# Kernel optimization log

Hardware: AMD Instinct MI355X
Metric: run time of the kernel (lower is better)

Reference implementation:

```python
import jax, jax.numpy as jnp
import numpy as np

_EPS = 1e-5
RC = 5.0   # cutoff radius
L = 20     # number of radial basis functions
N = 10000  # nodes
E = 100000 # edges
F = 128    # in_feats


def _ssp(x):
    # ShiftedSoftplus: softplus(x) - log(2)
    return jax.nn.softplus(x) - jnp.log(2.0)


def _rbf(r):
    # DimeNet radial basis: sqrt(2/rc) * sin(n*pi*r/rc) / r, n = 1..L.  r: [E,1] -> [E,L]
    n = jnp.arange(1, L + 1, dtype=r.dtype)
    return jnp.sqrt(2.0 / RC) * jnp.sin(n * jnp.pi * r / RC) / r


def _fc(u):
    # cosine cutoff applied elementwise: 0.5*(cos(pi*u/rc)+1) for u < rc else 0
    return jnp.where(u < RC, 0.5 * (jnp.cos(jnp.pi * u / RC) + 1.0), 0.0)


def setup_inputs() -> dict:
    key = jax.random.key(0)
    ks = jax.random.split(key, 12)

    def nrm(k, shape, scale=1.0):
        return jax.random.normal(k, shape, dtype=jnp.float32) * scale

    return {
        "x": nrm(ks[0], (N, 3)) * 3.0,           # atomic positions
        "v": nrm(ks[1], (N, F, 3)),               # vector node features
        "s": nrm(ks[2], (N, F)),                  # scalar node features
        "ms1_w": nrm(ks[3], (F, F), F ** -0.5),
        "ms1_b": jnp.zeros((F,), jnp.float32),
        "ms2_w": nrm(ks[4], (3 * F, F), F ** -0.5),
        "ms2_b": jnp.zeros((3 * F,), jnp.float32),
        "mv_w": nrm(ks[5], (3 * F, L), L ** -0.5),
        "mv_b": jnp.zeros((3 * F,), jnp.float32),
        "us1_w": nrm(ks[6], (F, F), F ** -0.5),
        "us1_b": jnp.zeros((F,), jnp.float32),
        "us2_w": nrm(ks[7], (3 * F, F), F ** -0.5),
        "us2_b": jnp.zeros((3 * F,), jnp.float32),
        "src": jax.random.randint(ks[8], (E,), 0, N, dtype=jnp.int32),
        "dst": jax.random.randint(ks[9], (E,), 0, N, dtype=jnp.int32),
    }


def reference(x, v, s, ms1_w, ms1_b, ms2_w, ms2_b, mv_w, mv_b,
              us1_w, us1_b, us2_w, us2_b, src, dst):
    # ---------- pass 1: message1 + reduce1 (sum over incoming edges) ----------
    sj = s[src]                                   # [E,F]   src scalar features
    vj = v[src]                                   # [E,F,3] src vector features
    vec = x[src] - x[dst]                         # [E,3]   x_i - x_j (molecule branch)
    r = jnp.sqrt(jnp.sum(vec ** 2, axis=-1) + _EPS)[:, None]          # [E,1]
    phi = _ssp(sj @ ms1_w.T + ms1_b) @ ms2_w.T + ms2_b                 # [E,3F]
    w = _fc(_rbf(r) @ mv_w.T + mv_b)                                    # [E,3F]
    v_, s_, r_ = jnp.split(phi * w, 3, axis=-1)                         # each [E,F]
    dv_e = vj * v_[:, :, None] + r_[:, :, None] * (vec / r)[:, None, :] # [E,F,3]
    dv = jax.ops.segment_sum(dv_e, dst, num_segments=N)                 # [N,F,3]
    ds = jax.ops.segment_sum(s_, dst, num_segments=N)                   # [N,F]
    v_new = v + dv
    s_new = s + ds

    # ---------- pass 2: message2 + reduce2 (mean over incoming edges) ----------
    s2 = _ssp(s_new[src] @ us1_w.T + us1_b) @ us2_w.T + us2_b           # [E,3F]
    deg = jax.ops.segment_sum(jnp.ones((E,), s.dtype), dst, num_segments=N)
    denom = jnp.maximum(deg, 1.0)
    s_mean = jax.ops.segment_sum(s2, dst, num_segments=N) / denom[:, None]        # [N,3F]
    uv = jax.ops.segment_sum(v_new[src], dst, num_segments=N) / denom[:, None, None]  # [N,F,3]
    avv, asv, ass = jnp.split(s_mean, 3, axis=-1)                       # each [N,F]
    norm = jnp.sqrt(jnp.sum(uv ** 2, axis=-1) + _EPS)[..., None]        # [N,F,1]
    dv2 = uv * avv[:, :, None]                                           # [N,F,3]
    ds2 = jnp.sum((uv / norm) ** 2, axis=-1) * asv + ass                 # [N,F]
    return (v_new + dv2, s_new + ds2)
```

## Files before the change

### kernel.cpp

```cpp
#include <hip/hip_runtime.h>
#include <hip/hip_bf16.h>


#define F_DIM   128
#define F3_DIM  384
#define L_DIM   20
#define CAP     64

typedef __attribute__((ext_vector_type(8))) short short8;
typedef __attribute__((ext_vector_type(4))) float f32x4;
typedef __attribute__((ext_vector_type(4))) unsigned short us4;

struct u3 { unsigned a, b, c; };

__device__ __forceinline__ unsigned short f2bf(float f) {
  union { float f; unsigned u; } a; a.f = f;
  unsigned u = a.u;
  u = (u + 0x7FFFu + ((u >> 16) & 1u)) >> 16;
  return (unsigned short)u;
}
__device__ __forceinline__ float bf2f(unsigned short u) {
  union { unsigned u; float f; } a; a.u = ((unsigned)u) << 16;
  return a.f;
}

__global__ __launch_bounds__(256) void cast_fill_kernel(
    const float* __restrict__ ms1_w, unsigned short* __restrict__ w_ms1,
    const float* __restrict__ ms2_w, unsigned short* __restrict__ w_ms2,
    const float* __restrict__ us1_w, unsigned short* __restrict__ w_us1,
    const float* __restrict__ us2_w, unsigned short* __restrict__ w_us2,
    const float* __restrict__ s,     unsigned short* __restrict__ sbf,
    const float* __restrict__ v,     us4* __restrict__ v4,
    const float* __restrict__ mv_w,  unsigned short* __restrict__ mvwB,
    const int* __restrict__ src, const int* __restrict__ dst,
    int* __restrict__ cursor, int* __restrict__ jbuf,
    int nF, int E)
{
  int i = blockIdx.x * 256 + threadIdx.x;
  if (i < 16384) w_ms1[i] = f2bf(ms1_w[i]);
  if (i < 49152) w_ms2[i] = f2bf(ms2_w[i]);
  if (i < 16384) w_us1[i] = f2bf(us1_w[i]);
  if (i < 49152) w_us2[i] = f2bf(us2_w[i]);
  if (i < nF)    sbf[i] = f2bf(s[i]);
  if (i < nF) {
    const float* vp = v + (size_t)i * 3;
    us4 o; o.x = f2bf(vp[0]); o.y = f2bf(vp[1]); o.z = f2bf(vp[2]); o.w = 0;
    v4[i] = o;
  }
  if (i < 384 * 32) {
    int o = i >> 5, k = i & 31;
    float val = (k < 20) ? mv_w[o * 20 + k] * 0.6324555320336759f : 0.f;
    mvwB[i] = f2bf(val);
  }
  if (i < E) {
    int d = dst[i];
    int p = atomicAdd(&cursor[d], 1);
    if (p < CAP) jbuf[d * CAP + p] = src[i];
  }
}

__global__ __launch_bounds__(64) void mlp_kernel(
    const unsigned short* __restrict__ X,
    const unsigned short* __restrict__ W1,
    const float* __restrict__ B1,
    const unsigned short* __restrict__ W2,
    const float* __restrict__ B2,
    const us4* __restrict__ Vin,
    unsigned short* __restrict__ Yc)
{
  __shared__ float HT[128 * 17];
  const int lane = threadIdx.x;
  const int c    = lane & 15;
  const int quad = lane >> 4;
  const int m0   = blockIdx.x * 16;

  f32x4 acc[8];
#pragma unroll
  for (int t = 0; t < 8; t++) acc[t] = (f32x4){0.f, 0.f, 0.f, 0.f};
#pragma unroll
  for (int kk = 0; kk < 4; kk++) {
    short8 a = *(const short8*)(X + (size_t)(m0 + c) * 128 + kk * 32 + quad * 8);
#pragma unroll
    for (int t = 0; t < 8; t++) {
      short8 b = *(const short8*)(W1 + (size_t)(t * 16 + c) * 128 + kk * 32 + quad * 8);
      acc[t] = __builtin_amdgcn_mfma_f32_16x16x32_bf16(a, b, acc[t], 0, 0, 0);
    }
  }
#pragma unroll
  for (int t = 0; t < 8; t++) {
    float bias = B1[t * 16 + c];
    int k = t * 16 + c;
#pragma unroll
    for (int r = 0; r < 4; r++) {
      float h = acc[t][r] + bias;
      float sp = (h > 15.f) ? h : log1pf(__expf(h));
      sp -= 0.69314718056f;
      HT[k * 17 + quad * 4 + r] = sp;
    }
  }
  __syncthreads();

  f32x4 acc2[3][8];
#pragma unroll
  for (int g = 0; g < 3; g++)
#pragma unroll
    for (int t = 0; t < 8; t++) acc2[g][t] = (f32x4){0.f, 0.f, 0.f, 0.f};
#pragma unroll
  for (int kk = 0; kk < 4; kk++) {
    short8 afr;
#pragma unroll
    for (int j = 0; j < 8; j++) {
      float hv = HT[(kk * 32 + quad * 8 + j) * 17 + c];
      afr[j] = (short)f2bf(hv);
    }
#pragma unroll
    for (int g = 0; g < 3; g++)
#pragma unroll
      for (int t = 0; t < 8; t++) {
        short8 b = *(const short8*)(W2 + (size_t)(g * 128 + t * 16 + c) * 128 + kk * 32 + quad * 8);
        acc2[g][t] = __builtin_amdgcn_mfma_f32_16x16x32_bf16(afr, b, acc2[g][t], 0, 0, 0);
      }
  }
#pragma unroll
  for (int t = 0; t < 8; t++) {
    int f = t * 16 + c;
    float b0 = B2[f], b1 = B2[128 + f], b2 = B2[256 + f];
#pragma unroll
    for (int r = 0; r < 4; r++) {
      int m = quad * 4 + r;
      us4 vv = Vin[(size_t)(m0 + m) * 128 + f];
      unsigned p0 = f2bf(acc2[0][t][r] + b0);
      unsigned p1 = f2bf(acc2[1][t][r] + b1);
      unsigned p2 = f2bf(acc2[2][t][r] + b2);
      u3 rec;
      rec.a = p0 | (p1 << 16);
      rec.b = p2 | ((unsigned)vv.x << 16);
      rec.c = (unsigned)vv.y | ((unsigned)vv.z << 16);
      *(u3*)(Yc + ((size_t)(m0 + m) * 128 + f) * 6) = rec;
    }
  }
}

__global__ __launch_bounds__(256, 4) void pass1_kernel(
    const float* __restrict__ x,
    const unsigned short* __restrict__ combo1,
    const float* __restrict__ v,
    const float* __restrict__ s,
    const unsigned short* __restrict__ mvwB,
    const float* __restrict__ mv_b,
    const int* __restrict__ jbuf,
    const int* __restrict__ deg,
    float* __restrict__ vnew, us4* __restrict__ vnew4,
    float* __restrict__ snew, unsigned short* __restrict__ snew_bf, int nNodes)
{
  __shared__ unsigned short Asn[32 * 32];
  __shared__ float4 Au[32];
  __shared__ us4 Wl[32 * 128];
  __shared__ float red[512];

  const int tid  = threadIdx.x;
  const int wave = tid >> 6, lane = tid & 63;
  const int half = wave >> 1, split = wave & 1;
  const int i = blockIdx.x;
  const int f = lane + 64 * half;
  const int c = lane & 15, quad = lane >> 4;

  int cnt = deg[i]; if (cnt > CAP) cnt = CAP;
  const int base = i * CAP;

  short8 bfr[6]; float bias[6];
#pragma unroll
  for (int p = 0; p < 3; p++)
#pragma unroll
    for (int h = 0; h < 2; h++) {
      int t = 2 * wave + h + 8 * p;
      bfr[p * 2 + h]  = *(const short8*)(mvwB + (size_t)(t * 16 + c) * 32 + quad * 8);
      bias[p * 2 + h] = mv_b[t * 16 + c];
    }

  const float xi0 = x[i * 3], xi1 = x[i * 3 + 1], xi2 = x[i * 3 + 2];
  int jv = (lane < cnt) ? jbuf[base + lane] : 0;

  float accV0 = 0.f, accV1 = 0.f, accV2 = 0.f, accS = 0.f;

  for (int bs = 0; bs < cnt; bs += 32) {
    int bcnt = cnt - bs; if (bcnt > 32) bcnt = 32;
    __syncthreads();

    if (tid < 32) {
      int e = bs + tid;
      int j = __shfl(jv, e);
      if (e < cnt) {
        float d0 = x[j * 3]     - xi0;
        float d1 = x[j * 3 + 1] - xi1;
        float d2 = x[j * 3 + 2] - xi2;
        float r = sqrtf(d0 * d0 + d1 * d1 + d2 * d2 + 1e-5f);
        float invr = 1.0f / r;
        Au[tid] = make_float4(d0 * invr, d1 * invr, d2 * invr, invr);
        float theta = r * 0.6283185307179586f;
        float s1, c1;
        __sincosf(theta, &s1, &c1);
        float c2 = 2.f * c1;
        float pm2 = s1, pm1 = c2 * s1;
        Asn[tid * 32 + 0] = f2bf(pm2);
        Asn[tid * 32 + 1] = f2bf(pm1);
#pragma unroll
        for (int l = 2; l < L_DIM; l++) {
          float cur = c2 * pm1 - pm2;
          Asn[tid * 32 + l] = f2bf(cur);
          pm2 = pm1; pm1 = cur;
        }
#pragma unroll
        for (int l = L_DIM; l < 32; l++) Asn[tid * 32 + l] = 0;
      }
    }
    __syncthreads();

    int nrg = (bcnt + 15) >> 4;
    for (int rg = 0; rg < nrg; rg++) {
      short8 a = *(const short8*)&Asn[(rg * 16 + c) * 32 + quad * 8];
      f32x4 acc[6];
#pragma unroll
      for (int q = 0; q < 6; q++)
        acc[q] = __builtin_amdgcn_mfma_f32_16x16x32_bf16(
            a, bfr[q], (f32x4){0.f, 0.f, 0.f, 0.f}, 0, 0, 0);
#pragma unroll
      for (int r = 0; r < 4; r++) {
        int el = rg * 16 + quad * 4 + r;
        if (el < bcnt) {
          float invr = Au[el].w;
#pragma unroll
          for (int h = 0; h < 2; h++) {
            float wp0 = fmaf(acc[h][r],     invr, bias[h]);
            float wp1 = fmaf(acc[2 + h][r], invr, bias[2 + h]);
            float wp2 = fmaf(acc[4 + h][r], invr, bias[4 + h]);
            float w0 = (wp0 < 5.f) ? 0.5f * (__cosf(wp0 * 0.6283185307179586f) + 1.f) : 0.f;
            float w1 = (wp1 < 5.f) ? 0.5f * (__cosf(wp1 * 0.6283185307179586f) + 1.f) : 0.f;
            float w2 = (wp2 < 5.f) ? 0.5f * (__cosf(wp2 * 0.6283185307179586f) + 1.f) : 0.f;
            us4 o; o.x = f2bf(w0); o.y = f2bf(w1); o.z = f2bf(w2); o.w = 0;
            Wl[el * 128 + wave * 32 + h * 16 + c] = o;
          }
        }
      }
    }
    __syncthreads();

    for (int e = split; e < bcnt; e += 2) {
      int j = __shfl(jv, bs + e);
      float4 u = Au[e];
      us4 wv = Wl[e * 128 + f];
      u3 cb = *(const u3*)(combo1 + ((size_t)j * 128 + f) * 6);
      float ph0 = bf2f((unsigned short)(cb.a & 0xffff));
      float ph1 = bf2f((unsigned short)(cb.a >> 16));
      float ph2 = bf2f((unsigned short)(cb.b & 0xffff));
      float vx  = bf2f((unsigned short)(cb.b >> 16));
      float vy  = bf2f((unsigned short)(cb.c & 0xffff));
      float vz  = bf2f((unsigned short)(cb.c >> 16));
      float m0 = ph0 * bf2f(wv.x);
      float m1 = ph1 * bf2f(wv.y);
      float m2 = ph2 * bf2f(wv.z);
      accV0 = fmaf(vx, m0, fmaf(m2, u.x, accV0));
      accV1 = fmaf(vy, m0, fmaf(m2, u.y, accV1));
      accV2 = fmaf(vz, m0, fmaf(m2, u.z, accV2));
      accS += m1;
    }
  }

  const int idx = half * 64 + lane;
  __syncthreads();
  if (split == 1) {
    red[idx * 4 + 0] = accV0; red[idx * 4 + 1] = accV1;
    red[idx * 4 + 2] = accV2; red[idx * 4 + 3] = accS;
  }
  __syncthreads();
  if (split == 0) {
    accV0 += red[idx * 4 + 0]; accV1 += red[idx * 4 + 1];
    accV2 += red[idx * 4 + 2]; accS  += red[idx * 4 + 3];
    size_t b3 = (size_t)i * 384 + f * 3;
    float n0 = v[b3] + accV0, n1 = v[b3 + 1] + accV1, n2 = v[b3 + 2] + accV2;
    vnew[b3] = n0; vnew[b3 + 1] = n1; vnew[b3 + 2] = n2;
    us4 o; o.x = f2bf(n0); o.y = f2bf(n1); o.z = f2bf(n2); o.w = 0;
    vnew4[(size_t)i * 128 + f] = o;
    size_t b1 = (size_t)i * 128 + f;
    float sv = s[b1] + accS;
    snew[b1] = sv;
    snew_bf[b1] = f2bf(sv);
  }
}

__global__ __launch_bounds__(256, 8) void pass2_kernel(
    const float* __restrict__ vnew,
    const float* __restrict__ snew,
    const unsigned short* __restrict__ combo2,
    const int* __restrict__ jbuf, const int* __restrict__ deg,
    float* __restrict__ vout, float* __restrict__ sout, int nNodes)
{
  __shared__ float red[1024];
  const int wave = threadIdx.x >> 6, lane = threadIdx.x & 63;
  const int half = wave >> 1, split = wave & 1;
  const int i = blockIdx.x;
  const int f = lane + 64 * half;

  int cnt = deg[i]; if (cnt > CAP) cnt = CAP;
  const int base = i * CAP;
  int jv = (lane < cnt) ? jbuf[base + lane] : 0;

  float accU0 = 0.f, accU1 = 0.f, accU2 = 0.f;
  float accM0 = 0.f, accM1 = 0.f, accM2 = 0.f;

#pragma unroll 2
  for (int e = split; e < cnt; e += 2) {
    int j = __shfl(jv, e);
    u3 cb = *(const u3*)(combo2 + ((size_t)j * 128 + f) * 6);
    accM0 += bf2f((unsigned short)(cb.a & 0xffff));
    accM1 += bf2f((unsigned short)(cb.a >> 16));
    accM2 += bf2f((unsigned short)(cb.b & 0xffff));
    accU0 += bf2f((unsigned short)(cb.b >> 16));
    accU1 += bf2f((unsigned short)(cb.c & 0xffff));
    accU2 += bf2f((unsigned short)(cb.c >> 16));
  }

  const int idx = half * 64 + lane;
  if (split == 1) {
    red[idx * 8 + 0] = accU0; red[idx * 8 + 1] = accU1; red[idx * 8 + 2] = accU2;
    red[idx * 8 + 3] = accM0; red[idx * 8 + 4] = accM1; red[idx * 8 + 5] = accM2;
  }
  __syncthreads();
  if (split == 0) {
    accU0 += red[idx * 8 + 0]; accU1 += red[idx * 8 + 1]; accU2 += red[idx * 8 + 2];
    accM0 += red[idx * 8 + 3]; accM1 += red[idx * 8 + 4]; accM2 += red[idx * 8 + 5];

    float dinv = 1.0f / (float)(cnt > 0 ? cnt : 1);
    float uv0 = accU0 * dinv, uv1 = accU1 * dinv, uv2 = accU2 * dinv;
    float avv = accM0 * dinv, asv = accM1 * dinv, ass = accM2 * dinv;
    float q = uv0 * uv0 + uv1 * uv1 + uv2 * uv2;
    float ds2 = (q / (q + 1e-5f)) * asv + ass;
    size_t b3 = (size_t)i * 384 + f * 3;
    vout[b3]     = vnew[b3]     + uv0 * avv;
    vout[b3 + 1] = vnew[b3 + 1] + uv1 * avv;
    vout[b3 + 2] = vnew[b3 + 2] + uv2 * avv;
    size_t b1 = (size_t)i * 128 + f;
    sout[b1] = snew[b1] + ds2;
  }
}

extern "C" void kernel_launch(void* const* d_in, const int* in_sizes, int n_in,
                              void* d_out, int out_size, void* d_ws, size_t ws_size,
                              hipStream_t stream)
{
  const float* x     = (const float*)d_in[0];
  const float* v     = (const float*)d_in[1];
  const float* s     = (const float*)d_in[2];
  const float* ms1_w = (const float*)d_in[3];
  const float* ms1_b = (const float*)d_in[4];
  const float* ms2_w = (const float*)d_in[5];
  const float* ms2_b = (const float*)d_in[6];
  const float* mv_w  = (const float*)d_in[7];
  const float* mv_b  = (const float*)d_in[8];
  const float* us1_w = (const float*)d_in[9];
  const float* us1_b = (const float*)d_in[10];
  const float* us2_w = (const float*)d_in[11];
  const float* us2_b = (const float*)d_in[12];
  const int*   src   = (const int*)d_in[13];
  const int*   dst   = (const int*)d_in[14];

  const int N = in_sizes[0] / 3;
  const int E = in_sizes[13];

  char* p = (char*)d_ws;
  auto alloc = [&](size_t bytes) -> void* {
    void* r = (void*)p;
    p += (bytes + 255) & ~(size_t)255;
    return r;
  };
  unsigned short* sbf   = (unsigned short*)alloc((size_t)N * 128 * 2);
  unsigned short* snbf  = (unsigned short*)alloc((size_t)N * 128 * 2);
  unsigned short* w_ms1 = (unsigned short*)alloc(16384 * 2);
  unsigned short* w_ms2 = (unsigned short*)alloc(49152 * 2);
  unsigned short* w_us1 = (unsigned short*)alloc(16384 * 2);
  unsigned short* w_us2 = (unsigned short*)alloc(49152 * 2);
  unsigned short* mvwB  = (unsigned short*)alloc(384 * 32 * 2);
  us4*   v4     = (us4*)alloc((size_t)N * 128 * 8);
  us4*   vnew4  = (us4*)alloc((size_t)N * 128 * 8);
  unsigned short* combo1 = (unsigned short*)alloc((size_t)N * 128 * 12);
  unsigned short* combo2 = (unsigned short*)alloc((size_t)N * 128 * 12);
  float* vnew   = (float*)alloc((size_t)N * 384 * 4);
  float* snew   = (float*)alloc((size_t)N * 128 * 4);
  int* cursor   = (int*)alloc((size_t)N * 4);
  int* jbuf     = (int*)alloc((size_t)N * CAP * 4);

  hipMemsetAsync(cursor, 0, (size_t)N * 4, stream);

  cast_fill_kernel<<<(N * 128 + 255) / 256, 256, 0, stream>>>(
      ms1_w, w_ms1, ms2_w, w_ms2, us1_w, w_us1, us2_w, w_us2,
      s, sbf, v, v4, mv_w, mvwB, src, dst, cursor, jbuf, N * 128, E);

  mlp_kernel<<<N / 16, 64, 0, stream>>>(sbf, w_ms1, ms1_b, w_ms2, ms2_b,
                                        v4, combo1);

  pass1_kernel<<<N, 256, 0, stream>>>(x, combo1, v, s, mvwB, mv_b,
                                      jbuf, cursor, vnew, vnew4, snew, snbf, N);

  mlp_kernel<<<N / 16, 64, 0, stream>>>(snbf, w_us1, us1_b, w_us2, us2_b,
                                        vnew4, combo2);

  float* vout = (float*)d_out;
  float* sout = vout + (size_t)N * 384;
  pass2_kernel<<<N, 256, 0, stream>>>(vnew, snew, combo2, jbuf, cursor,
                                      vout, sout, N);
}
```

Baseline: 248.2 us.

## Batch gather loads in edge loops and shrink pass1 edge batch for occupancy

Pass1 now processes edges in batches of 16 instead of 32, which halves its shared-memory footprint and lets the launch bound rise from 4 to 6 blocks per CU. The gather loop in both pass1 and pass2 issues up to 8 independent combo loads into registers before consuming them, so memory latency overlaps across edges. The extra in-flight registers and the tighter launch bound may cause spills, and smaller batches mean more syncthreads per node.

```diff
diff --git a/kernel.cpp b/kernel.cpp
--- a/kernel.cpp
+++ b/kernel.cpp
@@ -6,6 +6,7 @@
 #define F3_DIM  384
 #define L_DIM   20
 #define CAP     64
+#define BATCH   16
 
 typedef __attribute__((ext_vector_type(8))) short short8;
 typedef __attribute__((ext_vector_type(4))) float f32x4;
@@ -141,7 +142,7 @@
   }
 }
 
-__global__ __launch_bounds__(256, 4) void pass1_kernel(
+__global__ __launch_bounds__(256, 6) void pass1_kernel(
     const float* __restrict__ x,
     const unsigned short* __restrict__ combo1,
     const float* __restrict__ v,
@@ -153,9 +154,9 @@
     float* __restrict__ vnew, us4* __restrict__ vnew4,
     float* __restrict__ snew, unsigned short* __restrict__ snew_bf, int nNodes)
 {
-  __shared__ unsigned short Asn[32 * 32];
-  __shared__ float4 Au[32];
-  __shared__ us4 Wl[32 * 128];
+  __shared__ unsigned short Asn[BATCH * 32];
+  __shared__ float4 Au[BATCH];
+  __shared__ us4 Wl[BATCH * 128];
   __shared__ float red[512];
 
   const int tid  = threadIdx.x;
@@ -183,42 +184,42 @@
 
   float accV0 = 0.f, accV1 = 0.f, accV2 = 0.f, accS = 0.f;
 
-  for (int bs = 0; bs < cnt; bs += 32) {
-    int bcnt = cnt - bs; if (bcnt > 32) bcnt = 32;
+  for (int bs = 0; bs < cnt; bs += BATCH) {
+    int bcnt = cnt - bs; if (bcnt > BATCH) bcnt = BATCH;
     __syncthreads();
 
-    if (tid < 32) {
-      int e = bs + tid;
+    if (wave == 0) {
+      int t16 = lane & (BATCH - 1);
+      int e = bs + t16;
       int j = __shfl(jv, e);
-      if (e < cnt) {
+      if (lane < BATCH && e < cnt) {
         float d0 = x[j * 3]     - xi0;
         float d1 = x[j * 3 + 1] - xi1;
         float d2 = x[j * 3 + 2] - xi2;
         float r = sqrtf(d0 * d0 + d1 * d1 + d2 * d2 + 1e-5f);
         float invr = 1.0f / r;
-        Au[tid] = make_float4(d0 * invr, d1 * invr, d2 * invr, invr);
+        Au[lane] = make_float4(d0 * invr, d1 * invr, d2 * invr, invr);
         float theta = r * 0.6283185307179586f;
         float s1, c1;
         __sincosf(theta, &s1, &c1);
         float c2 = 2.f * c1;
         float pm2 = s1, pm1 = c2 * s1;
-        Asn[tid * 32 + 0] = f2bf(pm2);
-        Asn[tid * 32 + 1] = f2bf(pm1);
+        Asn[lane * 32 + 0] = f2bf(pm2);
+        Asn[lane * 32 + 1] = f2bf(pm1);
 #pragma unroll
         for (int l = 2; l < L_DIM; l++) {
           float cur = c2 * pm1 - pm2;
-          Asn[tid * 32 + l] = f2bf(cur);
+          Asn[lane * 32 + l] = f2bf(cur);
           pm2 = pm1; pm1 = cur;
         }
 #pragma unroll
-        for (int l = L_DIM; l < 32; l++) Asn[tid * 32 + l] = 0;
+        for (int l = L_DIM; l < 32; l++) Asn[lane * 32 + l] = 0;
       }
     }
     __syncthreads();
 
-    int nrg = (bcnt + 15) >> 4;
-    for (int rg = 0; rg < nrg; rg++) {
-      short8 a = *(const short8*)&Asn[(rg * 16 + c) * 32 + quad * 8];
+    {
+      short8 a = *(const short8*)&Asn[c * 32 + quad * 8];
       f32x4 acc[6];
 #pragma unroll
       for (int q = 0; q < 6; q++)
@@ -226,7 +227,7 @@
             a, bfr[q], (f32x4){0.f, 0.f, 0.f, 0.f}, 0, 0, 0);
 #pragma unroll
       for (int r = 0; r < 4; r++) {
-        int el = rg * 16 + quad * 4 + r;
+        int el = quad * 4 + r;
         if (el < bcnt) {
           float invr = Au[el].w;
 #pragma unroll
@@ -245,24 +246,35 @@
     }
     __syncthreads();
 
-    for (int e = split; e < bcnt; e += 2) {
-      int j = __shfl(jv, bs + e);
-      float4 u = Au[e];
-      us4 wv = Wl[e * 128 + f];
-      u3 cb = *(const u3*)(combo1 + ((size_t)j * 128 + f) * 6);
-      float ph0 = bf2f((unsigned short)(cb.a & 0xffff));
-      float ph1 = bf2f((unsigned short)(cb.a >> 16));
-      float ph2 = bf2f((unsigned short)(cb.b & 0xffff));
-      float vx  = bf2f((unsigned short)(cb.b >> 16));
-      float vy  = bf2f((unsigned short)(cb.c & 0xffff));
-      float vz  = bf2f((unsigned short)(cb.c >> 16));
-      float m0 = ph0 * bf2f(wv.x);
-      float m1 = ph1 * bf2f(wv.y);
-      float m2 = ph2 * bf2f(wv.z);
-      accV0 = fmaf(vx, m0, fmaf(m2, u.x, accV0));
-      accV1 = fmaf(vy, m0, fmaf(m2, u.y, accV1));
-      accV2 = fmaf(vz, m0, fmaf(m2, u.z, accV2));
-      accS += m1;
+    u3 cb[8];
+#pragma unroll
+    for (int k = 0; k < 8; k++) {
+      int e = split + 2 * k;
+      if (e < bcnt) {
+        int j = __shfl(jv, bs + e);
+        cb[k] = *(const u3*)(combo1 + ((size_t)j * 128 + f) * 6);
+      }
+    }
+#pragma unroll
+    for (int k = 0; k < 8; k++) {
+      int e = split + 2 * k;
+      if (e < bcnt) {
+        float4 u = Au[e];
+        us4 wv = Wl[e * 128 + f];
+        float ph0 = bf2f((unsigned short)(cb[k].a & 0xffff));
+        float ph1 = bf2f((unsigned short)(cb[k].a >> 16));
+        float ph2 = bf2f((unsigned short)(cb[k].b & 0xffff));
+        float vx  = bf2f((unsigned short)(cb[k].b >> 16));
+        float vy  = bf2f((unsigned short)(cb[k].c & 0xffff));
+        float vz  = bf2f((unsigned short)(cb[k].c >> 16));
+        float m0 = ph0 * bf2f(wv.x);
+        float m1 = ph1 * bf2f(wv.y);
+        float m2 = ph2 * bf2f(wv.z);
+        accV0 = fmaf(vx, m0, fmaf(m2, u.x, accV0));
+        accV1 = fmaf(vy, m0, fmaf(m2, u.y, accV1));
+        accV2 = fmaf(vz, m0, fmaf(m2, u.z, accV2));
+        accS += m1;
+      }
     }
   }
 
@@ -308,16 +320,28 @@
   float accU0 = 0.f, accU1 = 0.f, accU2 = 0.f;
   float accM0 = 0.f, accM1 = 0.f, accM2 = 0.f;
 
-#pragma unroll 2
-  for (int e = split; e < cnt; e += 2) {
-    int j = __shfl(jv, e);
-    u3 cb = *(const u3*)(combo2 + ((size_t)j * 128 + f) * 6);
-    accM0 += bf2f((unsigned short)(cb.a & 0xffff));
-    accM1 += bf2f((unsigned short)(cb.a >> 16));
-    accM2 += bf2f((unsigned short)(cb.b & 0xffff));
-    accU0 += bf2f((unsigned short)(cb.b >> 16));
-    accU1 += bf2f((unsigned short)(cb.c & 0xffff));
-    accU2 += bf2f((unsigned short)(cb.c >> 16));
+  for (int b0 = split; b0 < cnt; b0 += 16) {
+    u3 cb[8];
+#pragma unroll
+    for (int k = 0; k < 8; k++) {
+      int e = b0 + 2 * k;
+      if (e < cnt) {
+        int j = __shfl(jv, e);
+        cb[k] = *(const u3*)(combo2 + ((size_t)j * 128 + f) * 6);
+      }
+    }
+#pragma unroll
+    for (int k = 0; k < 8; k++) {
+      int e = b0 + 2 * k;
+      if (e < cnt) {
+        accM0 += bf2f((unsigned short)(cb[k].a & 0xffff));
+        accM1 += bf2f((unsigned short)(cb[k].a >> 16));
+        accM2 += bf2f((unsigned short)(cb[k].b & 0xffff));
+        accU0 += bf2f((unsigned short)(cb[k].b >> 16));
+        accU1 += bf2f((unsigned short)(cb[k].c & 0xffff));
+        accU2 += bf2f((unsigned short)(cb[k].c >> 16));
+      }
+    }
   }
 
   const int idx = half * 64 + lane;
```

Measured after the change: 380.7 us. +53.3%, slower.
